# Optimization experiments

Measured on AMD Instinct MI355X. Metric: run time of the kernel, lower is better.

Reference implementation:

```python
import jax, jax.numpy as jnp
import numpy as np

EPS = 1e-5
NUM_HEADS = 8
SPLIT = 7


def _ln(x, g, b):
    mu = jnp.mean(x, -1, keepdims=True)
    var = jnp.mean((x - mu) ** 2, -1, keepdims=True)
    return (x - mu) / jnp.sqrt(var + EPS) * g + b


def _lepe_attn(q, k, v, H, W, H_sp, W_sp, num_heads, conv_w, conv_b):
    # q,k,v: [B, H*W, C] (one branch, C = dim//2)
    B, L, C = q.shape
    d = C // num_heads
    scale = d ** -0.5
    nH, nW = H // H_sp, W // W_sp

    def to_win(t):  # [B,L,C] -> [B*nH*nW, heads, H_sp*W_sp, d]
        t = t.reshape(B, nH, H_sp, nW, W_sp, C).transpose(0, 1, 3, 2, 4, 5)
        return t.reshape(-1, H_sp * W_sp, num_heads, d).transpose(0, 2, 1, 3)

    qw, kw = to_win(q), to_win(k)

    # LePE: depthwise 3x3 conv on v inside each window (get_lepe)
    vimg = v.reshape(B, nH, H_sp, nW, W_sp, C).transpose(0, 1, 3, 2, 4, 5)
    vimg = vimg.reshape(-1, H_sp, W_sp, C)  # [nWin, H_sp, W_sp, C]
    lepe = jax.lax.conv_general_dilated(
        vimg, conv_w, (1, 1), 'SAME',
        dimension_numbers=('NHWC', 'HWIO', 'NHWC'),
        feature_group_count=C) + conv_b

    def img2heads(t):  # [nWin,H_sp,W_sp,C] -> [nWin, heads, N, d]
        return t.reshape(-1, H_sp * W_sp, num_heads, d).transpose(0, 2, 1, 3)

    vw = img2heads(vimg)
    lepe = img2heads(lepe)

    attn = jax.nn.softmax(jnp.einsum('whqd,whkd->whqk', qw * scale, kw), axis=-1)
    out = jnp.einsum('whqk,whkd->whqd', attn, vw) + lepe  # [nWin, heads, N, d]

    # windows2img
    out = out.transpose(0, 2, 1, 3).reshape(B, nH, nW, H_sp, W_sp, C)
    out = out.transpose(0, 1, 3, 2, 4, 5).reshape(B, H * W, C)
    return out


def setup_inputs() -> dict:
    key = jax.random.key(0)
    ks = jax.random.split(key, 12)
    B, H, W, C = 8, 56, 56, 256
    hid = 4 * C
    Cb = C // 2  # per-branch channels
    s = 0.02
    return {
        'x': jax.random.normal(ks[0], (B, H * W, C), jnp.float32),
        'H': H,
        'W': W,
        'norm1_g': jnp.ones((C,), jnp.float32),
        'norm1_b': jnp.zeros((C,), jnp.float32),
        'qkv_w': jax.random.normal(ks[1], (C, 3 * C), jnp.float32) * s,
        'proj_w': jax.random.normal(ks[2], (C, C), jnp.float32) * s,
        'proj_b': jnp.zeros((C,), jnp.float32),
        'conv0_w': jax.random.normal(ks[3], (3, 3, 1, Cb), jnp.float32) * s,
        'conv0_b': jnp.zeros((Cb,), jnp.float32),
        'conv1_w': jax.random.normal(ks[4], (3, 3, 1, Cb), jnp.float32) * s,
        'conv1_b': jnp.zeros((Cb,), jnp.float32),
        'norm2_g': jnp.ones((C,), jnp.float32),
        'norm2_b': jnp.zeros((C,), jnp.float32),
        'fc1_w': jax.random.normal(ks[5], (C, hid), jnp.float32) * s,
        'fc1_b': jnp.zeros((hid,), jnp.float32),
        'fc2_w': jax.random.normal(ks[6], (hid, C), jnp.float32) * s,
        'fc2_b': jnp.zeros((C,), jnp.float32),
    }


def reference(x, H, W, norm1_g, norm1_b, qkv_w, proj_w, proj_b,
              conv0_w, conv0_b, conv1_w, conv1_b,
              norm2_g, norm2_b, fc1_w, fc1_b, fc2_w, fc2_b):
    B, L, C = x.shape
    img = _ln(x, norm1_g, norm1_b)
    qkv = (img @ qkv_w).reshape(B, L, 3, C).transpose(2, 0, 1, 3)  # [3,B,L,C]
    h = C // 2
    # branch 0 (idx=0): full-height stripes; branch 1 (idx=1): full-width stripes
    x1 = _lepe_attn(qkv[0, :, :, :h], qkv[1, :, :, :h], qkv[2, :, :, :h],
                    H, W, H, SPLIT, NUM_HEADS // 2, conv0_w, conv0_b)
    x2 = _lepe_attn(qkv[0, :, :, h:], qkv[1, :, :, h:], qkv[2, :, :, h:],
                    H, W, SPLIT, W, NUM_HEADS // 2, conv1_w, conv1_b)
    att = jnp.concatenate([x1, x2], axis=2) @ proj_w + proj_b
    x = x + att
    y = _ln(x, norm2_g, norm2_b)
    y = jax.nn.gelu(y @ fc1_w + fc1_b, approximate=False) @ fc2_w + fc2_b
    return x + y
```

## Files before the change

kernel.cpp:

```cpp
#include <hip/hip_runtime.h>
#include <hip/hip_bf16.h>
#include <math.h>

constexpr int C_DIM = 256;
constexpr int MROWS = 25088;
constexpr int HID   = 1024;

typedef float  f32x4 __attribute__((ext_vector_type(4)));
typedef short  s16x8 __attribute__((ext_vector_type(8)));

__device__ __forceinline__ ushort f2bf(float f) {
    __hip_bfloat16 h = __float2bfloat16(f);
    return *reinterpret_cast<ushort*>(&h);
}
__device__ __forceinline__ unsigned pkbf2(float a, float b) {
    __hip_bfloat162 h = __float22bfloat162_rn(float2{a, b});
    return *reinterpret_cast<unsigned*>(&h);
}
__device__ __forceinline__ float bf2f(ushort u) {
    return __uint_as_float(((unsigned)u) << 16);
}

__device__ __forceinline__ float fast_gelu(float v) {
    float u = v * (0.7978845608028654f + 0.035677408136f * v * v);
    float e = __expf(2.0f * u);
    float t = 1.0f - 2.0f / (e + 1.0f);
    return 0.5f * v * (1.0f + t);
}

typedef const __attribute__((address_space(1))) unsigned guint;
typedef __attribute__((address_space(3))) unsigned luint;
__device__ __forceinline__ void gload16(const void* g, void* l) {
    __builtin_amdgcn_global_load_lds((guint*)g, (luint*)l, 16, 0, 0);
}

__global__ __launch_bounds__(256) void ln_kernel(
    const float* __restrict__ x, const float* __restrict__ g,
    const float* __restrict__ b, ushort* __restrict__ out)
{
    int wv = threadIdx.x >> 6, lane = threadIdx.x & 63;
    size_t row = (size_t)blockIdx.x * 4 + wv;
    float4 v = *(const float4*)(x + row * 256 + lane * 4);
    float s1 = v.x + v.y + v.z + v.w;
    float s2 = v.x*v.x + v.y*v.y + v.z*v.z + v.w*v.w;
    #pragma unroll
    for (int d = 1; d < 64; d <<= 1) {
        s1 += __shfl_xor(s1, d);
        s2 += __shfl_xor(s2, d);
    }
    float mu  = s1 * (1.0f / 256.0f);
    float var = s2 * (1.0f / 256.0f) - mu * mu;
    float inv = rsqrtf(var + 1e-5f);
    float4 gv = *(const float4*)(g + lane * 4);
    float4 bv = *(const float4*)(b + lane * 4);
    uint2 o;
    o.x = pkbf2((v.x - mu) * inv * gv.x + bv.x, (v.y - mu) * inv * gv.y + bv.y);
    o.y = pkbf2((v.z - mu) * inv * gv.z + bv.z, (v.w - mu) * inv * gv.w + bv.w);
    *(uint2*)(out + row * 256 + lane * 4) = o;
}

__global__ __launch_bounds__(256) void wcvt_all(
    const float* __restrict__ w0, const float* __restrict__ w1,
    const float* __restrict__ w2, const float* __restrict__ w3,
    ushort* __restrict__ o0, ushort* __restrict__ o1,
    ushort* __restrict__ o2, ushort* __restrict__ o3)
{
    __shared__ ushort tile[64][65];
    int bid = blockIdx.x;
    const float* w; ushort* o; int K, N, tIdx;
    if (bid < 48)       { w = w0; o = o0; K = 256;  N = 768;  tIdx = bid; }
    else if (bid < 64)  { w = w1; o = o1; K = 256;  N = 256;  tIdx = bid - 48; }
    else if (bid < 128) { w = w2; o = o2; K = 256;  N = 1024; tIdx = bid - 64; }
    else                { w = w3; o = o3; K = 1024; N = 256;  tIdx = bid - 128; }
    int nx = N >> 6;
    int bx = tIdx % nx, by = tIdx / nx;
    int n0 = bx * 64, k0 = by * 64;
    int c = threadIdx.x & 63, rr = threadIdx.x >> 6;
    #pragma unroll
    for (int i = 0; i < 64; i += 4) {
        int r = i + rr;
        tile[r][c] = f2bf(w[(size_t)(k0 + r) * N + n0 + c]);
    }
    __syncthreads();
    #pragma unroll
    for (int i = 0; i < 64; i += 4) {
        int r = i + rr;
        o[(size_t)(n0 + r) * K + k0 + c] = tile[c][r];
    }
}

template<int FUSE>
__global__ __launch_bounds__(256) void gemm_bf16(
    const ushort* __restrict__ A, const ushort* __restrict__ Bt,
    const float* __restrict__ bias, const float* res,
    void* Cout, int M, int N, int K, int NBX)
{
    __shared__ __align__(16) ushort As[3][128 * 32];
    __shared__ __align__(16) ushort Bs[3][128 * 32];
    int tid  = threadIdx.x;
    int lane = tid & 63, wv = tid >> 6;
    int lr = lane & 15, lg = lane >> 4;

    int nwg = gridDim.x;
    int qc = nwg >> 3, rc = nwg & 7;
    int xcd = blockIdx.x & 7, pos = blockIdx.x >> 3;
    int wg = (xcd < rc ? xcd * (qc + 1) : rc * (qc + 1) + (xcd - rc) * qc) + pos;
    int row0 = (wg / NBX) * 128, col0 = (wg % NBX) * 128;
    int wr = wv >> 1, wc = wv & 1;

    f32x4 acc[4][4];
    #pragma unroll
    for (int n = 0; n < 4; ++n)
        #pragma unroll
        for (int m = 0; m < 4; ++m)
            acc[n][m] = (f32x4){0.f, 0.f, 0.f, 0.f};

    int srow = wv * 32 + (lane >> 2);
    const ushort* gA  = A  + (size_t)(row0 + srow) * K + (lane & 3) * 8;
    const ushort* gA2 = gA + (size_t)16 * K;
    const ushort* gB  = Bt + (size_t)(col0 + srow) * K + (lane & 3) * 8;
    const ushort* gB2 = gB + (size_t)16 * K;

    auto stage = [&](int buf, int k0) {
        gload16(gA  + k0, &As[buf][(wv * 32 +  0) * 32]);
        gload16(gA2 + k0, &As[buf][(wv * 32 + 16) * 32]);
        gload16(gB  + k0, &Bs[buf][(wv * 32 +  0) * 32]);
        gload16(gB2 + k0, &Bs[buf][(wv * 32 + 16) * 32]);
    };

    const int NSTEP = K >> 5;
    stage(0, 0);
    stage(1, 32);
    asm volatile("s_waitcnt vmcnt(4)\n\ts_barrier" ::: "memory");

    for (int i = 0; i < NSTEP; ++i) {
        int cur = i % 3;
        const ushort* as = As[cur];
        const ushort* bs = Bs[cur];
        s16x8 af[4], bfg[4];
        #pragma unroll
        for (int m = 0; m < 4; ++m)
            af[m] = *(const s16x8*)&as[(wr * 64 + m * 16 + lr) * 32 + lg * 8];
        #pragma unroll
        for (int n = 0; n < 4; ++n)
            bfg[n] = *(const s16x8*)&bs[(wc * 64 + n * 16 + lr) * 32 + lg * 8];
        if (i + 2 < NSTEP) stage((i + 2) % 3, (i + 2) * 32);
        #pragma unroll
        for (int n = 0; n < 4; ++n)
            #pragma unroll
            for (int m = 0; m < 4; ++m)
                acc[n][m] = __builtin_amdgcn_mfma_f32_16x16x32_bf16(
                    bfg[n], af[m], acc[n][m], 0, 0, 0);
        if (i + 2 < NSTEP)
            asm volatile("s_waitcnt vmcnt(4)\n\ts_barrier" ::: "memory");
        else if (i + 1 < NSTEP)
            asm volatile("s_waitcnt vmcnt(0)\n\ts_barrier" ::: "memory");
    }

    int grow0 = row0 + wr * 64;
    int gcol0 = col0 + wc * 64;
    #pragma unroll
    for (int n = 0; n < 4; ++n) {
        int gcol = gcol0 + n * 16 + lg * 4;
        float4 b4 = make_float4(0.f, 0.f, 0.f, 0.f);
        if (FUSE >= 1) b4 = *(const float4*)&bias[gcol];
        #pragma unroll
        for (int m = 0; m < 4; ++m) {
            int grow = grow0 + m * 16 + lr;
            float v0 = acc[n][m][0] + b4.x;
            float v1 = acc[n][m][1] + b4.y;
            float v2 = acc[n][m][2] + b4.z;
            float v3 = acc[n][m][3] + b4.w;
            if (FUSE == 2) {
                v0 = fast_gelu(v0); v1 = fast_gelu(v1);
                v2 = fast_gelu(v2); v3 = fast_gelu(v3);
            }
            if (FUSE == 1) {
                const float4 rr = *(const float4*)&res[(size_t)grow * N + gcol];
                float4 o = make_float4(v0 + rr.x, v1 + rr.y, v2 + rr.z, v3 + rr.w);
                *(float4*)&((float*)Cout)[(size_t)grow * N + gcol] = o;
            } else {
                uint2 o;
                o.x = pkbf2(v0, v1);
                o.y = pkbf2(v2, v3);
                *(uint2*)&((ushort*)Cout)[(size_t)grow * N + gcol] = o;
            }
        }
    }
}

__device__ __forceinline__ int wrow(int branch, int b, int wi, int n) {
    if (branch) return b * 3136 + wi * 392 + n;
    int ii = n / 7;
    return b * 3136 + ii * 56 + wi * 7 + (n - ii * 7);
}

__global__ __launch_bounds__(512, 2) void attn_kernel(
    const ushort* __restrict__ qkv,
    const float* __restrict__ c0w, const float* __restrict__ c0b,
    const float* __restrict__ c1w, const float* __restrict__ c1b,
    ushort* __restrict__ att)
{
    __shared__ __align__(16) ushort Kh[2 * 400 * 16];
    __shared__ __align__(16) ushort Vt[32][424];
    __shared__ float  CwS[9][32];
    __shared__ float  CbS[32];

    int bid    = blockIdx.x;
    int branch = bid >> 8;
    int rem    = bid & 255;
    int head   = rem & 3;
    int win    = rem >> 2;
    int b  = win >> 3, wi = win & 7;
    int c0 = branch * 128 + head * 32;
    const float* cw = branch ? c1w : c0w;
    const float* cb = branch ? c1b : c0b;
    int tid = threadIdx.x;

    if (tid < 288) {
        int tap = tid >> 5, d = tid & 31;
        CwS[tap][d] = cw[tap * 128 + head * 32 + d];
    } else if (tid < 320) {
        CbS[tid - 288] = cb[head * 32 + (tid - 288)];
    }
    for (int e = tid; e < 1600; e += 512) {
        int n = e >> 2, quad = e & 3;
        uint4 v = make_uint4(0u, 0u, 0u, 0u);
        if (n < 392) {
            int gr = wrow(branch, b, wi, n);
            v = *(const uint4*)(qkv + (size_t)gr * 768 + 256 + c0 + quad * 8);
        }
        int idx = ((quad >> 1) * 6400 + n * 16 + (quad & 1) * 8) ^ (((n >> 2) & 1) << 3);
        *(uint4*)&Kh[idx] = v;
    }
    for (int e = tid; e < 1568; e += 512) {
        int n = e >> 2, quad = e & 3;
        int gr = wrow(branch, b, wi, n);
        uint4 v = *(const uint4*)(qkv + (size_t)gr * 768 + 512 + c0 + quad * 8);
        const ushort* us = (const ushort*)&v;
        #pragma unroll
        for (int j = 0; j < 8; ++j) Vt[quad * 8 + j][n] = us[j];
    }
    for (int e = tid; e < 1024; e += 512) {
        int d = e >> 5, k = 392 + (e & 31);
        Vt[d][k] = 0;
    }
    __syncthreads();

    int wv = tid >> 6, lane = tid & 63;
    int lr = lane & 15, lg = lane >> 4;
    constexpr float kSc = 0.17677669529663689f * 1.4426950408889634f;
    int Hsp = branch ? 7 : 56, Wsp = branch ? 56 : 7;
    int kidx = (((lg >> 1) * 6400) + lr * 16 + (lg & 1) * 8) ^ (((lr >> 2) & 1) << 3);
    const ushort* Kbase = &Kh[kidx];
    int sA = lr + ((2 * lg) & 3) * 16;
    int sB = lr + ((2 * lg + 1) & 3) * 16;
    bool loP = (lg < 2);

    for (int qt = wv; qt < 25; qt += 8) {
        int q0 = qt * 16;
        int qn = q0 + lr; if (qn > 391) qn = 391;
        int qr = wrow(branch, b, wi, qn);
        s16x8 qf = *(const s16x8*)(qkv + (size_t)qr * 768 + c0 + lg * 8);

        f32x4 o0 = {0.f, 0.f, 0.f, 0.f}, o1 = {0.f, 0.f, 0.f, 0.f};
        float psum = 0.0f;

        auto do_chunk = [&](int c, bool last) {
            f32x4 z = {0.f, 0.f, 0.f, 0.f};
            s16x8 kf0 = *(const s16x8*)&Kbase[c * 512];
            __builtin_amdgcn_s_setprio(1);
            f32x4 s0 = __builtin_amdgcn_mfma_f32_16x16x32_bf16(kf0, qf, z, 0, 0, 0);
            f32x4 s1 = z;
            if (!last) {
                s16x8 kf1 = *(const s16x8*)&Kbase[c * 512 + 256];
                s1 = __builtin_amdgcn_mfma_f32_16x16x32_bf16(kf1, qf, z, 0, 0, 0);
            }
            __builtin_amdgcn_s_setprio(0);
            float p0[4], p1[4];
            #pragma unroll
            for (int r = 0; r < 4; ++r) {
                p0[r] = exp2f(s0[r] * kSc);
                p1[r] = last ? 0.0f : exp2f(s1[r] * kSc);
            }
            if (last && !loP) {
                #pragma unroll
                for (int r = 0; r < 4; ++r) p0[r] = 0.0f;
            }
            #pragma unroll
            for (int r = 0; r < 4; ++r) psum += p0[r] + p1[r];
            unsigned A0 = pkbf2(p0[0], p0[1]), A1 = pkbf2(p0[2], p0[3]);
            unsigned B0 = pkbf2(p1[0], p1[1]), B1 = pkbf2(p1[2], p1[3]);
            unsigned a0A = __shfl(A0, sA), a1A = __shfl(A1, sA);
            unsigned b0A = __shfl(B0, sA), b1A = __shfl(B1, sA);
            unsigned a0B = __shfl(A0, sB), a1B = __shfl(A1, sB);
            unsigned b0B = __shfl(B0, sB), b1B = __shfl(B1, sB);
            union { unsigned u[4]; s16x8 v; } pu;
            pu.u[0] = loP ? a0A : b0A;
            pu.u[1] = loP ? a1A : b1A;
            pu.u[2] = loP ? a0B : b0B;
            pu.u[3] = loP ? a1B : b1B;
            s16x8 v0 = *(const s16x8*)&Vt[lr][c * 32 + lg * 8];
            s16x8 v1 = *(const s16x8*)&Vt[16 + lr][c * 32 + lg * 8];
            __builtin_amdgcn_s_setprio(1);
            o0 = __builtin_amdgcn_mfma_f32_16x16x32_bf16(pu.v, v0, o0, 0, 0, 0);
            o1 = __builtin_amdgcn_mfma_f32_16x16x32_bf16(pu.v, v1, o1, 0, 0, 0);
            __builtin_amdgcn_s_setprio(0);
        };

        for (int c = 0; c < 12; ++c) do_chunk(c, false);
        do_chunk(12, true);

        psum += __shfl_xor(psum, 16);
        psum += __shfl_xor(psum, 32);
        float linv[4];
        #pragma unroll
        for (int r = 0; r < 4; ++r)
            linv[r] = 1.0f / __shfl(psum, lg * 4 + r);
        #pragma unroll
        for (int r = 0; r < 4; ++r) { o0[r] *= linv[r]; o1[r] *= linv[r]; }

        #pragma unroll
        for (int r = 0; r < 4; ++r) {
            int q = q0 + lg * 4 + r;
            if (q >= 392) continue;
            int ii = branch ? (q / 56) : (q / 7);
            int jj = q - ii * Wsp;
            float a0 = o0[r], a1 = o1[r];
            #pragma unroll
            for (int kh = 0; kh < 3; ++kh) {
                int i2 = ii + kh - 1;
                if ((unsigned)i2 >= (unsigned)Hsp) continue;
                #pragma unroll
                for (int kw = 0; kw < 3; ++kw) {
                    int j2 = jj + kw - 1;
                    if ((unsigned)j2 >= (unsigned)Wsp) continue;
                    int pos = i2 * Wsp + j2;
                    a0 += CwS[kh * 3 + kw][lr]      * bf2f(Vt[lr][pos]);
                    a1 += CwS[kh * 3 + kw][16 + lr] * bf2f(Vt[16 + lr][pos]);
                }
            }
            a0 += CbS[lr]; a1 += CbS[16 + lr];
            int gr = wrow(branch, b, wi, q);
            att[(size_t)gr * 256 + branch * 128 + head * 32 + lr]      = f2bf(a0);
            att[(size_t)gr * 256 + branch * 128 + head * 32 + 16 + lr] = f2bf(a1);
        }
    }
}

extern "C" void kernel_launch(void* const* d_in, const int* in_sizes, int n_in,
                              void* d_out, int out_size, void* d_ws, size_t ws_size,
                              hipStream_t stream)
{
    const float* x      = (const float*)d_in[0];
    const float* n1g    = (const float*)d_in[3];
    const float* n1b    = (const float*)d_in[4];
    const float* qkv_w  = (const float*)d_in[5];
    const float* proj_w = (const float*)d_in[6];
    const float* proj_b = (const float*)d_in[7];
    const float* c0w    = (const float*)d_in[8];
    const float* c0b    = (const float*)d_in[9];
    const float* c1w    = (const float*)d_in[10];
    const float* c1b    = (const float*)d_in[11];
    const float* n2g    = (const float*)d_in[12];
    const float* n2b    = (const float*)d_in[13];
    const float* fc1_w  = (const float*)d_in[14];
    const float* fc1_b  = (const float*)d_in[15];
    const float* fc2_w  = (const float*)d_in[16];
    const float* fc2_b  = (const float*)d_in[17];
    float* out = (float*)d_out;

    char* ws = (char*)d_ws;
    const size_t SZ_BF = (size_t)MROWS * C_DIM * 2;
    ushort* img  = (ushort*)(ws);
    ushort* att  = (ushort*)(ws + SZ_BF);
    ushort* big  = (ushort*)(ws + 2 * SZ_BF);
    char*   wbase = ws + 2 * SZ_BF + (size_t)MROWS * HID * 2;
    ushort* qkvT = (ushort*)(wbase);
    ushort* projT= (ushort*)(wbase +  393216);
    ushort* fc1T = (ushort*)(wbase +  393216 + 131072);
    ushort* fc2T = (ushort*)(wbase +  393216 + 131072 + 524288);

    wcvt_all<<<192, 256, 0, stream>>>(qkv_w, proj_w, fc1_w, fc2_w, qkvT, projT, fc1T, fc2T);

    ln_kernel<<<MROWS / 4, 256, 0, stream>>>(x, n1g, n1b, img);
    gemm_bf16<0><<<196 * 6, 256, 0, stream>>>(
        img, qkvT, nullptr, nullptr, big, MROWS, 768, 256, 6);
    attn_kernel<<<512, 512, 0, stream>>>(big, c0w, c0b, c1w, c1b, att);
    gemm_bf16<1><<<196 * 2, 256, 0, stream>>>(
        att, projT, proj_b, x, out, MROWS, 256, 256, 2);
    ln_kernel<<<MROWS / 4, 256, 0, stream>>>(out, n2g, n2b, img);
    gemm_bf16<2><<<196 * 8, 256, 0, stream>>>(
        img, fc1T, fc1_b, nullptr, big, MROWS, HID, 256, 8);
    gemm_bf16<1><<<196 * 2, 256, 0, stream>>>(
        big, fc2T, fc2_b, out, out, MROWS, 256, 1024, 2);
}
```

Measured before the change: 274.0 us.

## Fuse LayerNorm2, fc1+GELU and fc2+residual into one MLP kernel

Replaces the LN2 kernel and the two MLP GEMM launches with a single kernel. Each 64-row block normalizes its rows into LDS, then computes fc1 in 128-wide hidden chunks, applies GELU into an LDS tile, and accumulates fc2 in registers before adding bias and residual. This removes the round trip of the 25088x1024 bf16 hidden activation and the normalized tensor through global memory. In exchange, B operands are read straight from global/L2 without LDS staging, each block handles only 64 rows (392 blocks), and the output is written in place over the residual input.

New measurement: 335.1 us. +22.3%, slower.

```diff
diff --git a/kernel.cpp b/kernel.cpp
--- a/kernel.cpp
+++ b/kernel.cpp
@@ -171,10 +171,6 @@
             float v1 = acc[n][m][1] + b4.y;
             float v2 = acc[n][m][2] + b4.z;
             float v3 = acc[n][m][3] + b4.w;
-            if (FUSE == 2) {
-                v0 = fast_gelu(v0); v1 = fast_gelu(v1);
-                v2 = fast_gelu(v2); v3 = fast_gelu(v3);
-            }
             if (FUSE == 1) {
                 const float4 rr = *(const float4*)&res[(size_t)grow * N + gcol];
                 float4 o = make_float4(v0 + rr.x, v1 + rr.y, v2 + rr.z, v3 + rr.w);
@@ -185,6 +181,142 @@
                 o.y = pkbf2(v2, v3);
                 *(uint2*)&((ushort*)Cout)[(size_t)grow * N + gcol] = o;
             }
+        }
+    }
+}
+
+__global__ __launch_bounds__(256, 2) void mlp_kernel(
+    const float* __restrict__ xr,
+    const float* __restrict__ n2g, const float* __restrict__ n2b,
+    const ushort* __restrict__ fc1T,
+    const float* __restrict__ fc1b,
+    const ushort* __restrict__ fc2T,
+    const float* __restrict__ fc2b,
+    float* __restrict__ out)
+{
+    __shared__ __align__(16) ushort Al[64 * 256];
+    __shared__ __align__(16) ushort Hl[64 * 136];
+
+    int tid = threadIdx.x, lane = tid & 63, wv = tid >> 6;
+    int lr = lane & 15, lg = lane >> 4;
+    int r0 = blockIdx.x * 64;
+
+    {
+        float4 gv = *(const float4*)&n2g[lane * 4];
+        float4 bv = *(const float4*)&n2b[lane * 4];
+        for (int it = 0; it < 16; ++it) {
+            int row = it * 4 + wv;
+            float4 v = *(const float4*)&xr[(size_t)(r0 + row) * 256 + lane * 4];
+            float s1 = v.x + v.y + v.z + v.w;
+            float s2 = v.x*v.x + v.y*v.y + v.z*v.z + v.w*v.w;
+            #pragma unroll
+            for (int d = 1; d < 64; d <<= 1) {
+                s1 += __shfl_xor(s1, d);
+                s2 += __shfl_xor(s2, d);
+            }
+            float mu  = s1 * (1.0f / 256.0f);
+            float var = s2 * (1.0f / 256.0f) - mu * mu;
+            float inv = rsqrtf(var + 1e-5f);
+            uint2 o;
+            o.x = pkbf2((v.x - mu) * inv * gv.x + bv.x, (v.y - mu) * inv * gv.y + bv.y);
+            o.y = pkbf2((v.z - mu) * inv * gv.z + bv.z, (v.w - mu) * inv * gv.w + bv.w);
+            int byteoff = (row * 512 + lane * 8) ^ ((row & 7) << 4);
+            *(uint2*)((char*)Al + byteoff) = o;
+        }
+    }
+    __syncthreads();
+
+    int wr = wv >> 1, wc = wv & 1;
+
+    f32x4 acc2[8][2];
+    #pragma unroll
+    for (int n = 0; n < 8; ++n)
+        #pragma unroll
+        for (int m = 0; m < 2; ++m)
+            acc2[n][m] = (f32x4){0.f, 0.f, 0.f, 0.f};
+
+    const ushort* pB1 = fc1T + (size_t)(wc * 64 + lr) * 256 + lg * 8;
+    const ushort* pB2 = fc2T + (size_t)(wc * 128 + lr) * 1024 + lg * 8;
+    int aswz = (lr & 7) << 4;
+
+    for (int c = 0; c < 8; ++c) {
+        f32x4 acc1[4][2];
+        #pragma unroll
+        for (int n = 0; n < 4; ++n)
+            #pragma unroll
+            for (int m = 0; m < 2; ++m)
+                acc1[n][m] = (f32x4){0.f, 0.f, 0.f, 0.f};
+        const ushort* b1p = pB1 + (size_t)c * 32768;
+        #pragma unroll
+        for (int kk = 0; kk < 8; ++kk) {
+            s16x8 af[2], bfg[4];
+            #pragma unroll
+            for (int m = 0; m < 2; ++m) {
+                int byteoff = ((wr * 32 + m * 16 + lr) * 512 + kk * 64 + lg * 16) ^ aswz;
+                af[m] = *(const s16x8*)((const char*)Al + byteoff);
+            }
+            #pragma unroll
+            for (int n = 0; n < 4; ++n)
+                bfg[n] = *(const s16x8*)&b1p[n * 4096 + kk * 32];
+            #pragma unroll
+            for (int n = 0; n < 4; ++n)
+                #pragma unroll
+                for (int m = 0; m < 2; ++m)
+                    acc1[n][m] = __builtin_amdgcn_mfma_f32_16x16x32_bf16(
+                        bfg[n], af[m], acc1[n][m], 0, 0, 0);
+        }
+        #pragma unroll
+        for (int n = 0; n < 4; ++n) {
+            float4 b1 = *(const float4*)&fc1b[c * 128 + wc * 64 + n * 16 + lg * 4];
+            #pragma unroll
+            for (int m = 0; m < 2; ++m) {
+                float v0 = fast_gelu(acc1[n][m][0] + b1.x);
+                float v1 = fast_gelu(acc1[n][m][1] + b1.y);
+                float v2 = fast_gelu(acc1[n][m][2] + b1.z);
+                float v3 = fast_gelu(acc1[n][m][3] + b1.w);
+                uint2 h;
+                h.x = pkbf2(v0, v1); h.y = pkbf2(v2, v3);
+                int row = wr * 32 + m * 16 + lr;
+                int col = wc * 64 + n * 16 + lg * 4;
+                *(uint2*)((char*)Hl + row * 272 + col * 2) = h;
+            }
+        }
+        __syncthreads();
+        const ushort* b2p = pB2 + c * 128;
+        #pragma unroll
+        for (int kk = 0; kk < 4; ++kk) {
+            s16x8 af2[2], bf2[8];
+            #pragma unroll
+            for (int m = 0; m < 2; ++m)
+                af2[m] = *(const s16x8*)((const char*)Hl +
+                          (wr * 32 + m * 16 + lr) * 272 + kk * 64 + lg * 16);
+            #pragma unroll
+            for (int n = 0; n < 8; ++n)
+                bf2[n] = *(const s16x8*)&b2p[(size_t)n * 16384 + kk * 32];
+            #pragma unroll
+            for (int n = 0; n < 8; ++n)
+                #pragma unroll
+                for (int m = 0; m < 2; ++m)
+                    acc2[n][m] = __builtin_amdgcn_mfma_f32_16x16x32_bf16(
+                        bf2[n], af2[m], acc2[n][m], 0, 0, 0);
+        }
+        __syncthreads();
+    }
+
+    #pragma unroll
+    for (int n = 0; n < 8; ++n) {
+        int col = wc * 128 + n * 16 + lg * 4;
+        float4 b2 = *(const float4*)&fc2b[col];
+        #pragma unroll
+        for (int m = 0; m < 2; ++m) {
+            size_t row = (size_t)(r0 + wr * 32 + m * 16 + lr);
+            float4 rr = *(const float4*)&xr[row * 256 + col];
+            float4 o;
+            o.x = acc2[n][m][0] + b2.x + rr.x;
+            o.y = acc2[n][m][1] + b2.y + rr.y;
+            o.z = acc2[n][m][2] + b2.z + rr.z;
+            o.w = acc2[n][m][3] + b2.w + rr.w;
+            *(float4*)&out[row * 256 + col] = o;
         }
     }
 }
@@ -389,9 +521,6 @@
     attn_kernel<<<512, 512, 0, stream>>>(big, c0w, c0b, c1w, c1b, att);
     gemm_bf16<1><<<196 * 2, 256, 0, stream>>>(
         att, projT, proj_b, x, out, MROWS, 256, 256, 2);
-    ln_kernel<<<MROWS / 4, 256, 0, stream>>>(out, n2g, n2b, img);
-    gemm_bf16<2><<<196 * 8, 256, 0, stream>>>(
-        img, fc1T, fc1_b, nullptr, big, MROWS, HID, 256, 8);
-    gemm_bf16<1><<<196 * 2, 256, 0, stream>>>(
-        big, fc2T, fc2_b, out, out, MROWS, 256, 1024, 2);
-}
+    mlp_kernel<<<MROWS / 64, 256, 0, stream>>>(
+        out, n2g, n2b, fc1T, fc1_b, fc2T, fc2_b, out);
+}
```
